# Kernel optimization log

Hardware: AMD Instinct MI355X
Metric: run time of the kernel (lower is better)

Reference implementation:

```python
import jax, jax.numpy as jnp
import numpy as np

N_NODES = 100000


def gcn_conv(x, src, dst, norm, W, b):
    # PyG GCNConv: linear transform first, then normalized scatter-add aggregation, then bias.
    xw = x @ W                                   # [N, out]
    msgs = xw[src] * norm[:, None]               # [E+N, out] gathered, degree-normalized messages
    out = jax.ops.segment_sum(msgs, dst, num_segments=N_NODES)
    return out + b


def _build_graph(edge_index):
    # add self-loops (PyG gcn_norm default)
    loop = jnp.arange(N_NODES, dtype=edge_index.dtype)
    src = jnp.concatenate([edge_index[0], loop])
    dst = jnp.concatenate([edge_index[1], loop])
    deg = jax.ops.segment_sum(jnp.ones_like(dst, dtype=jnp.float32), dst, num_segments=N_NODES)
    dis = jnp.where(deg > 0, jax.lax.rsqrt(jnp.maximum(deg, 1.0)), 0.0)
    norm = dis[src] * dis[dst]                   # D^-1/2 (A+I) D^-1/2 edge weights
    return src, dst, norm


def setup_inputs() -> dict:
    key = jax.random.key(0)
    ks = jax.random.split(key, 6)
    F_IN, H, C, E = 128, 128, 8, 1600000
    x = jax.random.normal(ks[0], (N_NODES, F_IN), dtype=jnp.float32)
    edge_index = jax.random.randint(ks[1], (2, E), 0, N_NODES, dtype=jnp.int64)
    # glorot-style init for conv weights
    W1 = jax.random.normal(ks[2], (F_IN, H), dtype=jnp.float32) * (1.0 / np.sqrt(F_IN))
    b1 = jnp.zeros((H,), dtype=jnp.float32)
    W2 = jax.random.normal(ks[3], (H, C), dtype=jnp.float32) * (1.0 / np.sqrt(H))
    b2 = jnp.zeros((C,), dtype=jnp.float32)
    return {"x": x, "edge_index": edge_index, "W1": W1, "b1": b1, "W2": W2, "b2": b2}


def reference(x, edge_index, W1, b1, W2, b2):
    src, dst, norm = _build_graph(edge_index)
    h = gcn_conv(x, src, dst, norm, W1, b1)
    h = jax.nn.relu(h)
    # dropout is identity in eval mode
    out = gcn_conv(h, src, dst, norm, W2, b2)
    return jax.nn.log_softmax(out, axis=1)
```

## Files before the change

### kernel.cpp

```cpp
#include <hip/hip_runtime.h>

#define N_NODES 100000
#define NBKT 782
#define EPB 8192
#define SL_STRIDE 800000

typedef unsigned int uint;
typedef __attribute__((ext_vector_type(8))) short bf16x8;
typedef __attribute__((ext_vector_type(4))) float f32x4;

union FragU { uint4 u; bf16x8 b; };

__device__ __forceinline__ uint pack_bf16_2(float a, float b) {
    uint ua = __float_as_uint(a), ub = __float_as_uint(b);
    ua += 0x7fff + ((ua >> 16) & 1);
    ub += 0x7fff + ((ub >> 16) & 1);
    return (ua >> 16) | (ub & 0xffff0000u);
}
__device__ __forceinline__ float bf_lo(uint u) { return __uint_as_float(u << 16); }
__device__ __forceinline__ float bf_hi(uint u) { return __uint_as_float(u & 0xffff0000u); }

__device__ __forceinline__ int edge_at(const int* __restrict__ ei, int idx, int is64) {
    return is64 ? ei[2 * idx] : ei[idx];
}

__global__ void k_zero(int* __restrict__ bkt_cnt, int* __restrict__ flag,
                       const int* __restrict__ ei, float4* __restrict__ y2q) {
    int i = blockIdx.x * 256 + threadIdx.x;
    if (i < NBKT) bkt_cnt[i] = 0;
    if (i < N_NODES * 2) y2q[i] = make_float4(0.f, 0.f, 0.f, 0.f);
    if (blockIdx.x == 0) {
        if (threadIdx.x == 0) flag[0] = 0;
        __syncthreads();
        int any = 0;
        for (int j = threadIdx.x; j < 4096; j += 256) any |= ei[2 * j + 1];
        if (any) atomicOr(flag, 1);
    }
}

__global__ __launch_bounds__(256) void kA1(const int* __restrict__ ei, int E,
                                           const int* __restrict__ flag,
                                           int* __restrict__ bkt_cnt) {
    __shared__ int h[NBKT];
    int t = threadIdx.x;
    for (int i = t; i < NBKT; i += 256) h[i] = 0;
    __syncthreads();
    int is64 = (flag[0] == 0);
    int base = blockIdx.x * EPB;
    int end = min(base + EPB, E);
    for (int e = base + t; e < end; e += 256) {
        int d = edge_at(ei, E + e, is64);
        atomicAdd(&h[d >> 7], 1);
    }
    __syncthreads();
    for (int i = t; i < NBKT; i += 256)
        if (h[i]) atomicAdd(&bkt_cnt[i], h[i]);
}

__global__ __launch_bounds__(1024) void kA2(const int* __restrict__ bkt_cnt,
                                            int* __restrict__ bkt_off,
                                            int* __restrict__ bkt_cursor) {
    __shared__ int s[1024];
    int t = threadIdx.x;
    int v = (t < NBKT) ? bkt_cnt[t] : 0;
    s[t] = v;
    __syncthreads();
    for (int d = 1; d < 1024; d <<= 1) {
        int y = (t >= d) ? s[t - d] : 0;
        __syncthreads();
        s[t] += y;
        __syncthreads();
    }
    if (t < NBKT) {
        int o = s[t] - v;
        bkt_off[t] = o;
        bkt_cursor[t] = o;
    }
}

__global__ __launch_bounds__(256) void kA3(const int* __restrict__ ei, int E,
                                           const int* __restrict__ flag,
                                           int* __restrict__ bkt_cursor,
                                           uint* __restrict__ bkt_data) {
    __shared__ int h[NBKT];
    __shared__ int base[NBKT];
    int t = threadIdx.x;
    for (int i = t; i < NBKT; i += 256) h[i] = 0;
    __syncthreads();
    int is64 = (flag[0] == 0);
    int lo = blockIdx.x * EPB;
    int end = min(lo + EPB, E);
    for (int e = lo + t; e < end; e += 256) {
        int d = edge_at(ei, E + e, is64);
        atomicAdd(&h[d >> 7], 1);
    }
    __syncthreads();
    for (int i = t; i < NBKT; i += 256) {
        int c = h[i];
        base[i] = c ? atomicAdd(&bkt_cursor[i], c) : 0;
    }
    __syncthreads();
    for (int i = t; i < NBKT; i += 256) h[i] = 0;
    __syncthreads();
    for (int e = lo + t; e < end; e += 256) {
        int d = edge_at(ei, E + e, is64);
        int s = edge_at(ei, e, is64);
        int b = d >> 7;
        int r = atomicAdd(&h[b], 1);
        bkt_data[base[b] + r] = ((uint)s << 7) | (uint)(d & 127);
    }
}

__global__ __launch_bounds__(256) void kB(const uint* __restrict__ bkt_data,
                                          const int* __restrict__ bkt_off,
                                          const int* __restrict__ bkt_cnt,
                                          int* __restrict__ srcs,
                                          int* __restrict__ count,
                                          int* __restrict__ offs,
                                          float* __restrict__ dis) {
    __shared__ int lc[128];
    __shared__ int sc[128];
    __shared__ int lcur[128];
    int t = threadIdx.x;
    int b = blockIdx.x;
    if (t < 128) { lc[t] = 0; lcur[t] = 0; }
    __syncthreads();
    int start = bkt_off[b];
    int n = bkt_cnt[b];
    for (int i = t; i < n; i += 256)
        atomicAdd(&lc[bkt_data[start + i] & 127], 1);
    __syncthreads();
    if (t < 128) sc[t] = lc[t];
    __syncthreads();
    for (int d = 1; d < 128; d <<= 1) {
        int y = 0;
        if (t < 128 && t >= d) y = sc[t - d];
        __syncthreads();
        if (t < 128) sc[t] += y;
        __syncthreads();
    }
    if (t < 128) {
        int node = b * 128 + t;
        if (node < N_NODES) {
            int c = lc[t];
            count[node] = c;
            offs[node] = start + sc[t] - c;
            dis[node] = rsqrtf((float)c + 1.0f);
        }
    }
    __syncthreads();
    for (int i = t; i < n; i += 256) {
        uint rec = bkt_data[start + i];
        int dl = rec & 127;
        int r = atomicAdd(&lcur[dl], 1);
        srcs[start + (sc[dl] - lc[dl]) + r] = rec >> 7;
    }
}

__global__ __launch_bounds__(256) void k_gemm1(const float* __restrict__ x,
                                               const float* __restrict__ W,
                                               const float* __restrict__ dis,
                                               uint* __restrict__ y1s) {
    __shared__ uint4 WtA[2048];
    char* wt = (char*)WtA;
    int t = threadIdx.x;

    const float4* W4 = (const float4*)W;
#pragma unroll
    for (int ii = 0; ii < 4; ++ii) {
        int tile = t + 256 * ii;
        int nq = tile >> 5, kq = tile & 31;
        float4 r0 = W4[(4 * kq + 0) * 32 + nq];
        float4 r1 = W4[(4 * kq + 1) * 32 + nq];
        float4 r2 = W4[(4 * kq + 2) * 32 + nq];
        float4 r3 = W4[(4 * kq + 3) * 32 + nq];
        const float* p0 = (const float*)&r0;
        const float* p1 = (const float*)&r1;
        const float* p2 = (const float*)&r2;
        const float* p3 = (const float*)&r3;
#pragma unroll
        for (int cc = 0; cc < 4; ++cc) {
            int n = 4 * nq + cc;
            uint2 v;
            v.x = pack_bf16_2(p0[cc], p1[cc]);
            v.y = pack_bf16_2(p2[cc], p3[cc]);
            *(uint2*)(wt + n * 256 + (((kq >> 1) ^ (n & 7)) << 4) + ((kq & 1) << 3)) = v;
        }
    }
    __syncthreads();

    int w = t >> 6, lane = t & 63;
    int m = lane & 15, kg = lane >> 4;
    int row0 = blockIdx.x * 64 + 16 * w;

    int arow = row0 + m;
    bool av = arow < N_NODES;
    const float4* xr = (const float4*)(x + (size_t)arow * 128);
    float4 z4 = make_float4(0.f, 0.f, 0.f, 0.f);
    FragU af[4];
#pragma unroll
    for (int kf = 0; kf < 4; ++kf) {
        float4 g0 = av ? xr[8 * kf + 2 * kg]     : z4;
        float4 g1 = av ? xr[8 * kf + 2 * kg + 1] : z4;
        const float* a0 = (const float*)&g0;
        const float* a1 = (const float*)&g1;
        af[kf].u.x = pack_bf16_2(a0[0], a0[1]);
        af[kf].u.y = pack_bf16_2(a0[2], a0[3]);
        af[kf].u.z = pack_bf16_2(a1[0], a1[1]);
        af[kf].u.w = pack_bf16_2(a1[2], a1[3]);
    }

    int crow = row0 + 4 * kg;
    float dd[4];
#pragma unroll
    for (int rr = 0; rr < 4; ++rr)
        dd[rr] = (crow + rr < N_NODES) ? dis[crow + rr] : 0.0f;

#pragma unroll
    for (int ct = 0; ct < 8; ++ct) {
        f32x4 acc = {0.f, 0.f, 0.f, 0.f};
#pragma unroll
        for (int kf = 0; kf < 4; ++kf) {
            int n = 16 * ct + m;
            bf16x8 bw = *(const bf16x8*)(wt + n * 256 + ((((kf << 2) | kg) ^ (n & 7)) << 4));
            acc = __builtin_amdgcn_mfma_f32_16x16x32_bf16(af[kf].b, bw, acc, 0, 0, 0);
        }
#pragma unroll
        for (int rr = 0; rr < 4; ++rr) {
            float v = acc[rr] * dd[rr];
            float p = __shfl_xor(v, 1, 64);
            if (!(lane & 1)) {
                int grow = crow + rr;
                if (grow < N_NODES)
                    y1s[(size_t)ct * SL_STRIDE + grow * 8 + (m >> 1)] = pack_bf16_2(v, p);
            }
        }
    }
}

__global__ __launch_bounds__(256) void k_agg1s(const uint* __restrict__ y1s,
                                               const int* __restrict__ srcs,
                                               const int* __restrict__ offs,
                                               const int* __restrict__ count,
                                               const float* __restrict__ dis,
                                               const float* __restrict__ b1,
                                               const float* __restrict__ W2,
                                               float* __restrict__ y2) {
    int t = threadIdx.x;
    int slice = blockIdx.x & 7;
    int nb = blockIdx.x >> 3;
    int g = t >> 3;
    int j = t & 7;
    int d = nb * 32 + g;

    float w0[8], w1[8];
    const float* wr0 = W2 + (size_t)(slice * 16 + 2 * j) * 8;
#pragma unroll
    for (int c = 0; c < 8; ++c) { w0[c] = wr0[c]; w1[c] = wr0[8 + c]; }

    const uint4* ybase = (const uint4*)(y1s + (size_t)slice * SL_STRIDE);
    float acc[16];
#pragma unroll
    for (int c = 0; c < 16; ++c) acc[c] = 0.0f;

    int st = offs[d], n = count[d];
    int i = j;
    for (; i + 8 <= n; i += 16) {
        int s0 = srcs[st + i];
        int s1 = (i + 8 < n) ? srcs[st + i + 8] : d;
        uint4 a0 = ybase[(size_t)s0 * 2];
        uint4 b0 = ybase[(size_t)s0 * 2 + 1];
        uint4 a1 = ybase[(size_t)s1 * 2];
        uint4 b1q = ybase[(size_t)s1 * 2 + 1];
        acc[0]  += bf_lo(a0.x) + bf_lo(a1.x);  acc[1]  += bf_hi(a0.x) + bf_hi(a1.x);
        acc[2]  += bf_lo(a0.y) + bf_lo(a1.y);  acc[3]  += bf_hi(a0.y) + bf_hi(a1.y);
        acc[4]  += bf_lo(a0.z) + bf_lo(a1.z);  acc[5]  += bf_hi(a0.z) + bf_hi(a1.z);
        acc[6]  += bf_lo(a0.w) + bf_lo(a1.w);  acc[7]  += bf_hi(a0.w) + bf_hi(a1.w);
        acc[8]  += bf_lo(b0.x) + bf_lo(b1q.x); acc[9]  += bf_hi(b0.x) + bf_hi(b1q.x);
        acc[10] += bf_lo(b0.y) + bf_lo(b1q.y); acc[11] += bf_hi(b0.y) + bf_hi(b1q.y);
        acc[12] += bf_lo(b0.z) + bf_lo(b1q.z); acc[13] += bf_hi(b0.z) + bf_hi(b1q.z);
        acc[14] += bf_lo(b0.w) + bf_lo(b1q.w); acc[15] += bf_hi(b0.w) + bf_hi(b1q.w);
    }
    if (i <= n) {
        int sk = (i < n) ? srcs[st + i] : d;
        uint4 a = ybase[(size_t)sk * 2];
        uint4 bq = ybase[(size_t)sk * 2 + 1];
        acc[0]  += bf_lo(a.x);  acc[1]  += bf_hi(a.x);
        acc[2]  += bf_lo(a.y);  acc[3]  += bf_hi(a.y);
        acc[4]  += bf_lo(a.z);  acc[5]  += bf_hi(a.z);
        acc[6]  += bf_lo(a.w);  acc[7]  += bf_hi(a.w);
        acc[8]  += bf_lo(bq.x); acc[9]  += bf_hi(bq.x);
        acc[10] += bf_lo(bq.y); acc[11] += bf_hi(bq.y);
        acc[12] += bf_lo(bq.z); acc[13] += bf_hi(bq.z);
        acc[14] += bf_lo(bq.w); acc[15] += bf_hi(bq.w);
    }

    int hi4 = (j >> 2) & 1, hi2 = (j >> 1) & 1, hi1 = j & 1;
    float v8[8];
#pragma unroll
    for (int c = 0; c < 8; ++c) {
        float keep = hi4 ? acc[c + 8] : acc[c];
        float send = hi4 ? acc[c] : acc[c + 8];
        v8[c] = keep + __shfl_xor(send, 4, 8);
    }
    float v4[4];
#pragma unroll
    for (int c = 0; c < 4; ++c) {
        float keep = hi2 ? v8[c + 4] : v8[c];
        float send = hi2 ? v8[c] : v8[c + 4];
        v4[c] = keep + __shfl_xor(send, 2, 8);
    }
    float v2[2];
#pragma unroll
    for (int c = 0; c < 2; ++c) {
        float keep = hi1 ? v4[c + 2] : v4[c];
        float send = hi1 ? v4[c] : v4[c + 2];
        v2[c] = keep + __shfl_xor(send, 1, 8);
    }

    float ddv = dis[d];
    float2 b = ((const float2*)b1)[slice * 8 + j];
    float h0 = fmaxf(fmaf(v2[0], ddv, b.x), 0.0f);
    float h1 = fmaxf(fmaf(v2[1], ddv, b.y), 0.0f);

    float p[8];
#pragma unroll
    for (int c = 0; c < 8; ++c) p[c] = h0 * w0[c] + h1 * w1[c];
    float q4[4];
#pragma unroll
    for (int c = 0; c < 4; ++c) {
        float keep = hi4 ? p[c + 4] : p[c];
        float send = hi4 ? p[c] : p[c + 4];
        q4[c] = keep + __shfl_xor(send, 4, 8);
    }
    float q2[2];
#pragma unroll
    for (int c = 0; c < 2; ++c) {
        float keep = hi2 ? q4[c + 2] : q4[c];
        float send = hi2 ? q4[c] : q4[c + 2];
        q2[c] = keep + __shfl_xor(send, 2, 8);
    }
    float keep = hi1 ? q2[1] : q2[0];
    float send = hi1 ? q2[0] : q2[1];
    float q = keep + __shfl_xor(send, 1, 8);

    atomicAdd(&y2[(size_t)d * 8 + j], q * ddv);
}

__global__ __launch_bounds__(256) void k_agg2(const float* __restrict__ y2,
                                              const int* __restrict__ srcs,
                                              const int* __restrict__ offs,
                                              const int* __restrict__ count,
                                              const float* __restrict__ dis,
                                              const float* __restrict__ b2,
                                              float* __restrict__ out) {
    int g = (blockIdx.x * 256 + threadIdx.x) >> 3;
    int c = threadIdx.x & 7;
    if (g >= N_NODES) return;
    float acc = y2[(size_t)g * 8 + c];
    float acc2 = 0.0f;
    int st = offs[g], n = count[g];
    int i = 0;
    for (; i + 2 <= n; i += 2) {
        int s0 = srcs[st + i], s1 = srcs[st + i + 1];
        acc  += y2[(size_t)s0 * 8 + c];
        acc2 += y2[(size_t)s1 * 8 + c];
    }
    if (i < n) acc += y2[(size_t)srcs[st + i] * 8 + c];
    acc += acc2;

    float o = fmaf(acc, dis[g], b2[c]);
    float m = o;
#pragma unroll
    for (int k = 1; k < 8; k <<= 1) m = fmaxf(m, __shfl_xor(m, k, 64));
    float e = expf(o - m);
    float ssum = e;
#pragma unroll
    for (int k = 1; k < 8; k <<= 1) ssum += __shfl_xor(ssum, k, 64);
    out[(size_t)g * 8 + c] = (o - m) - logf(ssum);
}

extern "C" void kernel_launch(void* const* d_in, const int* in_sizes, int n_in,
                              void* d_out, int out_size, void* d_ws, size_t ws_size,
                              hipStream_t stream) {
    const float* x  = (const float*)d_in[0];
    const int*   ei = (const int*)d_in[1];
    const float* W1 = (const float*)d_in[2];
    const float* b1 = (const float*)d_in[3];
    const float* W2 = (const float*)d_in[4];
    const float* b2 = (const float*)d_in[5];
    float* out = (float*)d_out;
    const int E = in_sizes[1] / 2;

    char* ws = (char*)d_ws;
    int*   flag       = (int*)ws;
    int*   bkt_cnt    = (int*)(ws + 256);
    int*   bkt_off    = bkt_cnt + 784;
    int*   bkt_cursor = bkt_off + 784;
    int*   count      = bkt_cursor + 784;
    int*   offs       = count + N_NODES;
    float* dis        = (float*)(offs + N_NODES);
    uint*  bkt_data   = (uint*)(dis + N_NODES);
    int*   srcs       = (int*)(bkt_data + E);
    uint*  y1s        = (uint*)(srcs + E);
    float* y2         = (float*)(y1s + (size_t)8 * SL_STRIDE);

    const int PB = (E + EPB - 1) / EPB;

    k_zero <<<782, 256, 0, stream>>>(bkt_cnt, flag, ei, (float4*)y2);
    kA1    <<<PB, 256, 0, stream>>>(ei, E, flag, bkt_cnt);
    kA2    <<<1, 1024, 0, stream>>>(bkt_cnt, bkt_off, bkt_cursor);
    kA3    <<<PB, 256, 0, stream>>>(ei, E, flag, bkt_cursor, bkt_data);
    kB     <<<NBKT, 256, 0, stream>>>(bkt_data, bkt_off, bkt_cnt, srcs, count, offs, dis);

    k_gemm1<<<(N_NODES + 63) / 64, 256, 0, stream>>>(x, W1, dis, y1s);
    k_agg1s<<<8 * 3125, 256, 0, stream>>>(y1s, srcs, offs, count, dis, b1, W2, y2);
    k_agg2 <<<(N_NODES + 31) / 32, 256, 0, stream>>>(y2, srcs, offs, count, dis, b2, out);
}
```

Before: 227.1 us.

## Drop zero kernel, use per-block histogram slab, add nontemporal loads/stores

Removes the k_zero launch by probing the edge dtype in each partition block, writing per-block bucket histograms to a slab that kA2 reduces, and moving the y2 zeroing into kB. It also adds nontemporal loads and stores in the GEMM and aggregation kernels and simplifies the agg1 inner loop from two-way to one-way unrolling, loading W2 after the loop. The aim is to cut launch count and global atomics and to reduce cache pollution. In exchange, each block repeats the dtype probe, kA2 serially sums about 196 slab rows, and the agg1 loop exposes less memory-level parallelism.

```diff
diff --git a/kernel.cpp b/kernel.cpp
--- a/kernel.cpp
+++ b/kernel.cpp
@@ -24,28 +24,25 @@
     return is64 ? ei[2 * idx] : ei[idx];
 }
 
-__global__ void k_zero(int* __restrict__ bkt_cnt, int* __restrict__ flag,
-                       const int* __restrict__ ei, float4* __restrict__ y2q) {
-    int i = blockIdx.x * 256 + threadIdx.x;
-    if (i < NBKT) bkt_cnt[i] = 0;
-    if (i < N_NODES * 2) y2q[i] = make_float4(0.f, 0.f, 0.f, 0.f);
-    if (blockIdx.x == 0) {
-        if (threadIdx.x == 0) flag[0] = 0;
-        __syncthreads();
-        int any = 0;
-        for (int j = threadIdx.x; j < 4096; j += 256) any |= ei[2 * j + 1];
-        if (any) atomicOr(flag, 1);
-    }
+__device__ __forceinline__ int block_probe_is64(const int* __restrict__ ei, int* sh) {
+    int t = threadIdx.x;
+    if (t == 0) *sh = 0;
+    __syncthreads();
+    int any = 0;
+    for (int j = t; j < 4096; j += blockDim.x) any |= ei[2 * j + 1];
+    if (any) atomicOr(sh, 1);
+    __syncthreads();
+    return (*sh == 0);
 }
 
 __global__ __launch_bounds__(256) void kA1(const int* __restrict__ ei, int E,
-                                           const int* __restrict__ flag,
-                                           int* __restrict__ bkt_cnt) {
+                                           int* __restrict__ slab) {
     __shared__ int h[NBKT];
-    int t = threadIdx.x;
+    __shared__ int shp;
+    int t = threadIdx.x;
+    int is64 = block_probe_is64(ei, &shp);
     for (int i = t; i < NBKT; i += 256) h[i] = 0;
     __syncthreads();
-    int is64 = (flag[0] == 0);
     int base = blockIdx.x * EPB;
     int end = min(base + EPB, E);
     for (int e = base + t; e < end; e += 256) {
@@ -54,15 +51,19 @@
     }
     __syncthreads();
     for (int i = t; i < NBKT; i += 256)
-        if (h[i]) atomicAdd(&bkt_cnt[i], h[i]);
-}
-
-__global__ __launch_bounds__(1024) void kA2(const int* __restrict__ bkt_cnt,
+        slab[(size_t)blockIdx.x * NBKT + i] = h[i];
+}
+
+__global__ __launch_bounds__(1024) void kA2(const int* __restrict__ slab, int PB,
+                                            int* __restrict__ bkt_cnt,
                                             int* __restrict__ bkt_off,
                                             int* __restrict__ bkt_cursor) {
     __shared__ int s[1024];
     int t = threadIdx.x;
-    int v = (t < NBKT) ? bkt_cnt[t] : 0;
+    int v = 0;
+    if (t < NBKT)
+        for (int b = 0; b < PB; ++b) v += slab[(size_t)b * NBKT + t];
+    if (t < NBKT) bkt_cnt[t] = v;
     s[t] = v;
     __syncthreads();
     for (int d = 1; d < 1024; d <<= 1) {
@@ -79,15 +80,15 @@
 }
 
 __global__ __launch_bounds__(256) void kA3(const int* __restrict__ ei, int E,
-                                           const int* __restrict__ flag,
                                            int* __restrict__ bkt_cursor,
                                            uint* __restrict__ bkt_data) {
     __shared__ int h[NBKT];
     __shared__ int base[NBKT];
-    int t = threadIdx.x;
+    __shared__ int shp;
+    int t = threadIdx.x;
+    int is64 = block_probe_is64(ei, &shp);
     for (int i = t; i < NBKT; i += 256) h[i] = 0;
     __syncthreads();
-    int is64 = (flag[0] == 0);
     int lo = blockIdx.x * EPB;
     int end = min(lo + EPB, E);
     for (int e = lo + t; e < end; e += 256) {
@@ -117,12 +118,18 @@
                                           int* __restrict__ srcs,
                                           int* __restrict__ count,
                                           int* __restrict__ offs,
-                                          float* __restrict__ dis) {
+                                          float* __restrict__ dis,
+                                          float* __restrict__ y2) {
     __shared__ int lc[128];
     __shared__ int sc[128];
     __shared__ int lcur[128];
     int t = threadIdx.x;
     int b = blockIdx.x;
+    {
+        int zb = b * 1024;
+        int ze = min(zb + 1024, N_NODES * 8);
+        for (int i = zb + t; i < ze; i += 256) y2[i] = 0.0f;
+    }
     if (t < 128) { lc[t] = 0; lcur[t] = 0; }
     __syncthreads();
     int start = bkt_off[b];
@@ -195,19 +202,17 @@
 
     int arow = row0 + m;
     bool av = arow < N_NODES;
-    const float4* xr = (const float4*)(x + (size_t)arow * 128);
-    float4 z4 = make_float4(0.f, 0.f, 0.f, 0.f);
+    const f32x4* xr = (const f32x4*)(x + (size_t)arow * 128);
+    f32x4 z4 = {0.f, 0.f, 0.f, 0.f};
     FragU af[4];
 #pragma unroll
     for (int kf = 0; kf < 4; ++kf) {
-        float4 g0 = av ? xr[8 * kf + 2 * kg]     : z4;
-        float4 g1 = av ? xr[8 * kf + 2 * kg + 1] : z4;
-        const float* a0 = (const float*)&g0;
-        const float* a1 = (const float*)&g1;
-        af[kf].u.x = pack_bf16_2(a0[0], a0[1]);
-        af[kf].u.y = pack_bf16_2(a0[2], a0[3]);
-        af[kf].u.z = pack_bf16_2(a1[0], a1[1]);
-        af[kf].u.w = pack_bf16_2(a1[2], a1[3]);
+        f32x4 g0 = av ? __builtin_nontemporal_load(&xr[8 * kf + 2 * kg])     : z4;
+        f32x4 g1 = av ? __builtin_nontemporal_load(&xr[8 * kf + 2 * kg + 1]) : z4;
+        af[kf].u.x = pack_bf16_2(g0[0], g0[1]);
+        af[kf].u.y = pack_bf16_2(g0[2], g0[3]);
+        af[kf].u.z = pack_bf16_2(g1[0], g1[1]);
+        af[kf].u.w = pack_bf16_2(g1[2], g1[3]);
     }
 
     int crow = row0 + 4 * kg;
@@ -232,7 +237,8 @@
             if (!(lane & 1)) {
                 int grow = crow + rr;
                 if (grow < N_NODES)
-                    y1s[(size_t)ct * SL_STRIDE + grow * 8 + (m >> 1)] = pack_bf16_2(v, p);
+                    __builtin_nontemporal_store(pack_bf16_2(v, p),
+                        &y1s[(size_t)ct * SL_STRIDE + grow * 8 + (m >> 1)]);
             }
         }
     }
@@ -253,37 +259,16 @@
     int j = t & 7;
     int d = nb * 32 + g;
 
-    float w0[8], w1[8];
-    const float* wr0 = W2 + (size_t)(slice * 16 + 2 * j) * 8;
-#pragma unroll
-    for (int c = 0; c < 8; ++c) { w0[c] = wr0[c]; w1[c] = wr0[8 + c]; }
-
     const uint4* ybase = (const uint4*)(y1s + (size_t)slice * SL_STRIDE);
     float acc[16];
 #pragma unroll
     for (int c = 0; c < 16; ++c) acc[c] = 0.0f;
 
     int st = offs[d], n = count[d];
-    int i = j;
-    for (; i + 8 <= n; i += 16) {
-        int s0 = srcs[st + i];
-        int s1 = (i + 8 < n) ? srcs[st + i + 8] : d;
-        uint4 a0 = ybase[(size_t)s0 * 2];
-        uint4 b0 = ybase[(size_t)s0 * 2 + 1];
-        uint4 a1 = ybase[(size_t)s1 * 2];
-        uint4 b1q = ybase[(size_t)s1 * 2 + 1];
-        acc[0]  += bf_lo(a0.x) + bf_lo(a1.x);  acc[1]  += bf_hi(a0.x) + bf_hi(a1.x);
-        acc[2]  += bf_lo(a0.y) + bf_lo(a1.y);  acc[3]  += bf_hi(a0.y) + bf_hi(a1.y);
-        acc[4]  += bf_lo(a0.z) + bf_lo(a1.z);  acc[5]  += bf_hi(a0.z) + bf_hi(a1.z);
-        acc[6]  += bf_lo(a0.w) + bf_lo(a1.w);  acc[7]  += bf_hi(a0.w) + bf_hi(a1.w);
-        acc[8]  += bf_lo(b0.x) + bf_lo(b1q.x); acc[9]  += bf_hi(b0.x) + bf_hi(b1q.x);
-        acc[10] += bf_lo(b0.y) + bf_lo(b1q.y); acc[11] += bf_hi(b0.y) + bf_hi(b1q.y);
-        acc[12] += bf_lo(b0.z) + bf_lo(b1q.z); acc[13] += bf_hi(b0.z) + bf_hi(b1q.z);
-        acc[14] += bf_lo(b0.w) + bf_lo(b1q.w); acc[15] += bf_hi(b0.w) + bf_hi(b1q.w);
-    }
-    if (i <= n) {
-        int sk = (i < n) ? srcs[st + i] : d;
-        uint4 a = ybase[(size_t)sk * 2];
+    for (int i = j; i <= n; i += 8) {
+        int sk = d;
+        if (i < n) sk = __builtin_nontemporal_load(&srcs[st + i]);
+        uint4 a  = ybase[(size_t)sk * 2];
         uint4 bq = ybase[(size_t)sk * 2 + 1];
         acc[0]  += bf_lo(a.x);  acc[1]  += bf_hi(a.x);
         acc[2]  += bf_lo(a.y);  acc[3]  += bf_hi(a.y);
@@ -323,9 +308,10 @@
     float h0 = fmaxf(fmaf(v2[0], ddv, b.x), 0.0f);
     float h1 = fmaxf(fmaf(v2[1], ddv, b.y), 0.0f);
 
+    const float* wr0 = W2 + (size_t)(slice * 16 + 2 * j) * 8;
     float p[8];
 #pragma unroll
-    for (int c = 0; c < 8; ++c) p[c] = h0 * w0[c] + h1 * w1[c];
+    for (int c = 0; c < 8; ++c) p[c] = h0 * wr0[c] + h1 * wr0[8 + c];
     float q4[4];
 #pragma unroll
     for (int c = 0; c < 4; ++c) {
@@ -362,11 +348,12 @@
     int st = offs[g], n = count[g];
     int i = 0;
     for (; i + 2 <= n; i += 2) {
-        int s0 = srcs[st + i], s1 = srcs[st + i + 1];
+        int s0 = __builtin_nontemporal_load(&srcs[st + i]);
+        int s1 = __builtin_nontemporal_load(&srcs[st + i + 1]);
         acc  += y2[(size_t)s0 * 8 + c];
         acc2 += y2[(size_t)s1 * 8 + c];
     }
-    if (i < n) acc += y2[(size_t)srcs[st + i] * 8 + c];
+    if (i < n) acc += y2[(size_t)__builtin_nontemporal_load(&srcs[st + i]) * 8 + c];
     acc += acc2;
 
     float o = fmaf(acc, dis[g], b2[c]);
@@ -391,27 +378,26 @@
     const float* b2 = (const float*)d_in[5];
     float* out = (float*)d_out;
     const int E = in_sizes[1] / 2;
-
-    char* ws = (char*)d_ws;
-    int*   flag       = (int*)ws;
-    int*   bkt_cnt    = (int*)(ws + 256);
+    const int PB = (E + EPB - 1) / EPB;
+    const int Epad = (E + 3) & ~3;
+    int slabInts = (PB * NBKT + 3) & ~3;
+
+    int*   slab       = (int*)d_ws;
+    int*   bkt_cnt    = slab + slabInts;
     int*   bkt_off    = bkt_cnt + 784;
     int*   bkt_cursor = bkt_off + 784;
     int*   count      = bkt_cursor + 784;
     int*   offs       = count + N_NODES;
     float* dis        = (float*)(offs + N_NODES);
     uint*  bkt_data   = (uint*)(dis + N_NODES);
-    int*   srcs       = (int*)(bkt_data + E);
-    uint*  y1s        = (uint*)(srcs + E);
+    int*   srcs       = (int*)(bkt_data + Epad);
+    uint*  y1s        = (uint*)(srcs + Epad);
     float* y2         = (float*)(y1s + (size_t)8 * SL_STRIDE);
 
-    const int PB = (E + EPB - 1) / EPB;
-
-    k_zero <<<782, 256, 0, stream>>>(bkt_cnt, flag, ei, (float4*)y2);
-    kA1    <<<PB, 256, 0, stream>>>(ei, E, flag, bkt_cnt);
-    kA2    <<<1, 1024, 0, stream>>>(bkt_cnt, bkt_off, bkt_cursor);
-    kA3    <<<PB, 256, 0, stream>>>(ei, E, flag, bkt_cursor, bkt_data);
-    kB     <<<NBKT, 256, 0, stream>>>(bkt_data, bkt_off, bkt_cnt, srcs, count, offs, dis);
+    kA1    <<<PB, 256, 0, stream>>>(ei, E, slab);
+    kA2    <<<1, 1024, 0, stream>>>(slab, PB, bkt_cnt, bkt_off, bkt_cursor);
+    kA3    <<<PB, 256, 0, stream>>>(ei, E, bkt_cursor, bkt_data);
+    kB     <<<NBKT, 256, 0, stream>>>(bkt_data, bkt_off, bkt_cnt, srcs, count, offs, dis, y2);
 
     k_gemm1<<<(N_NODES + 63) / 64, 256, 0, stream>>>(x, W1, dis, y1s);
     k_agg1s<<<8 * 3125, 256, 0, stream>>>(y1s, srcs, offs, count, dis, b1, W2, y2);
```

New measurement: 282.3 us. 1.24x slower.
